# Performance work log

Measured on AMD Instinct MI355X. Metric: run time of the kernel, lower is better.

The kernel has to match this reference:

```python
import jax, jax.numpy as jnp
import numpy as np

N_NODES = 50000
N_EDGES = 1600000
IN_FEAT = 128
OUT_FEAT = 32
N_HEADS = 4
NEG_SLOPE = 0.2


def setup_inputs() -> dict:
    key = jax.random.key(0)
    ks = jax.random.split(key, 7)
    h = jax.random.normal(ks[0], (N_NODES, IN_FEAT), dtype=jnp.float32)
    W = jax.random.normal(ks[1], (IN_FEAT, N_HEADS * OUT_FEAT), dtype=jnp.float32) * 0.05
    attn_l = jax.random.normal(ks[2], (N_HEADS, OUT_FEAT), dtype=jnp.float32) * 0.1
    attn_r = jax.random.normal(ks[3], (N_HEADS, OUT_FEAT), dtype=jnp.float32) * 0.1
    bias = jax.random.normal(ks[4], (N_HEADS * OUT_FEAT,), dtype=jnp.float32) * 0.01
    src = jax.random.randint(ks[5], (N_EDGES,), 0, N_NODES, dtype=jnp.int32)
    dst = jax.random.randint(ks[6], (N_EDGES,), 0, N_NODES, dtype=jnp.int32)
    return {"h": h, "W": W, "attn_l": attn_l, "attn_r": attn_r, "bias": bias, "src": src, "dst": dst}


def reference(h, W, attn_l, attn_r, bias, src, dst):
    N = h.shape[0]
    H, F = attn_l.shape
    # linear projection, [N, H, F]
    feat = (h @ W).reshape(N, H, F)
    # per-node attention halves
    el = jnp.einsum('nhf,hf->nh', feat, attn_l)  # [N, H]
    er = jnp.einsum('nhf,hf->nh', feat, attn_r)  # [N, H]
    # edge scores: e_ij = leaky_relu(el[src] + er[dst])
    e = jax.nn.leaky_relu(el[src] + er[dst], negative_slope=NEG_SLOPE)  # [E, H]
    # edge softmax over incoming edges of each dst node (numerically stable)
    m = jax.ops.segment_max(e, dst, num_segments=N)  # [N, H]
    m = jnp.where(jnp.isfinite(m), m, jnp.zeros_like(m))  # zero-in-degree guard
    ex = jnp.exp(e - m[dst])  # [E, H]
    denom = jax.ops.segment_sum(ex, dst, num_segments=N)  # [N, H]
    alpha = ex / jnp.maximum(denom[dst], 1e-9)  # [E, H]
    # weighted scatter-sum aggregation
    msg = feat[src] * alpha[:, :, None]  # [E, H, F]
    rst = jax.ops.segment_sum(msg, dst, num_segments=N)  # [N, H, F]
    rst = rst + bias.reshape(1, H, F)
    rst = jax.nn.relu(rst)
    # wrapper: norm=None, dropout=0.0 (eval), mean over heads
    return jnp.mean(rst, axis=1)  # [N, F]
```

## Files before the change

kernel.cpp:

```cpp
#include <hip/hip_runtime.h>
#include <hip/hip_bf16.h>
#include <hip/hip_fp16.h>
#include <math.h>


#define NEG_SLOPE 0.2f
#define HEADS 4
#define FEAT_OUT 32
#define FEAT_ALL 128
#define IN_FEAT 128
#define CAP 96
#define KP 136
#define NB_SC 2048

typedef _Float16 half8 __attribute__((ext_vector_type(8)));
typedef float float4v __attribute__((ext_vector_type(4)));
typedef unsigned int uint4v __attribute__((ext_vector_type(4)));

__device__ __forceinline__ float leaky(float v) {
    return v > 0.f ? v : NEG_SLOPE * v;
}

__global__ __launch_bounds__(256) void k1_fused(
    const int* __restrict__ src, const int* __restrict__ dst, int E,
    int* __restrict__ cnt, unsigned short* __restrict__ slots,
    const float* __restrict__ h, const float* __restrict__ W,
    const float* __restrict__ attn_l, const float* __restrict__ attn_r,
    unsigned char* __restrict__ feat8, float2* __restrict__ elsc,
    float* __restrict__ er, int N, int nG) {
    __shared__ _Float16 sf[64 * KP];
    const int t = threadIdx.x;

    if ((int)blockIdx.x >= nG) {
        const int b = blockIdx.x - nG;
        const int p = b & 7;
        const int g = b >> 3;
        const int NPER = (N + 7) >> 3;
        const int lo = p * NPER;
        const int hi = (lo + NPER < N) ? lo + NPER : N;
        const int tpp = (NB_SC >> 3) * 256;
        const int E4 = E & ~3;
        for (int e0 = (g * 256 + t) * 4; e0 < E4; e0 += tpp * 4) {
            uint4v d4 = *(const uint4v*)(dst + e0);
            bool need = false;
#pragma unroll
            for (int j = 0; j < 4; j++)
                need |= ((int)d4[j] >= lo && (int)d4[j] < hi);
            if (!need) continue;
            uint4v s4 = *(const uint4v*)(src + e0);
#pragma unroll
            for (int j = 0; j < 4; j++) {
                int d = (int)d4[j];
                if (d >= lo && d < hi) {
                    int pos = atomicAdd(&cnt[d], 1);
                    if (pos < CAP) slots[(size_t)d * CAP + pos] = (unsigned short)s4[j];
                }
            }
        }
        if (g == 0 && t < E - E4) {
            int e = E4 + t;
            int d = dst[e];
            if (d >= lo && d < hi) {
                int pos = atomicAdd(&cnt[d], 1);
                if (pos < CAP) slots[(size_t)d * CAP + pos] = (unsigned short)src[e];
            }
        }
        return;
    }

    const int n0 = blockIdx.x * 64;
    const int wv_ = t >> 6;
    const int lane = t & 63;
    const int m16 = lane & 15;
    const int quad = lane >> 4;
    const int rowA = wv_ * 16 + m16;
    int nA = n0 + rowA; if (nA > N - 1) nA = N - 1;
    const float* hp = h + (size_t)nA * IN_FEAT + quad * 8;

    float4v acc[8];
#pragma unroll
    for (int i = 0; i < 8; i++) acc[i] = (float4v){0.f, 0.f, 0.f, 0.f};

#pragma unroll
    for (int k0 = 0; k0 < 128; k0 += 32) {
        float4 a0 = *(const float4*)(hp + k0);
        float4 a1 = *(const float4*)(hp + k0 + 4);
        half8 a;
        a[0] = (_Float16)a0.x; a[1] = (_Float16)a0.y;
        a[2] = (_Float16)a0.z; a[3] = (_Float16)a0.w;
        a[4] = (_Float16)a1.x; a[5] = (_Float16)a1.y;
        a[6] = (_Float16)a1.z; a[7] = (_Float16)a1.w;
        const float* wp = W + (size_t)(k0 + quad * 8) * FEAT_ALL + m16;
#pragma unroll
        for (int tN = 0; tN < 8; tN++) {
            const float* wpt = wp + tN * 16;
            half8 b;
            b[0] = (_Float16)wpt[0];
            b[1] = (_Float16)wpt[FEAT_ALL];
            b[2] = (_Float16)wpt[2 * FEAT_ALL];
            b[3] = (_Float16)wpt[3 * FEAT_ALL];
            b[4] = (_Float16)wpt[4 * FEAT_ALL];
            b[5] = (_Float16)wpt[5 * FEAT_ALL];
            b[6] = (_Float16)wpt[6 * FEAT_ALL];
            b[7] = (_Float16)wpt[7 * FEAT_ALL];
            acc[tN] = __builtin_amdgcn_mfma_f32_16x16x32_f16(a, b, acc[tN], 0, 0, 0);
        }
    }

#pragma unroll
    for (int tN = 0; tN < 8; tN++)
#pragma unroll
        for (int r = 0; r < 4; r++) {
            int row = wv_ * 16 + quad * 4 + r;
            sf[row * KP + tN * 16 + m16] = (_Float16)acc[tN][r];
        }
    __syncthreads();

    {
        int r = t >> 2, hh = t & 3;
        int n = n0 + r;
        if (n < N) {
            const _Float16* sp_ = &sf[r * KP + hh * FEAT_OUT];
            float sl = 0.f, sr = 0.f, mx = 0.f;
#pragma unroll
            for (int f = 0; f < FEAT_OUT; f++) {
                float v = (float)sp_[f];
                sl += v * attn_l[hh * FEAT_OUT + f];
                sr += v * attn_r[hh * FEAT_OUT + f];
                mx = fmaxf(mx, fabsf(v));
            }
            er[n * HEADS + hh] = sr;
            elsc[n * HEADS + hh] = make_float2(sl, mx * (1.f / 127.f));
            const float inv = mx > 0.f ? 127.f / mx : 0.f;
            unsigned int w[8];
#pragma unroll
            for (int k2 = 0; k2 < 8; k2++) {
                unsigned int wv = 0;
#pragma unroll
                for (int j = 0; j < 4; j++) {
                    float v = (float)sp_[k2 * 4 + j];
                    int q = __float2int_rn(v * inv);
                    wv |= ((unsigned int)(q & 0xff)) << (8 * j);
                }
                w[k2] = wv;
            }
            uint4* dp = (uint4*)(feat8 + (size_t)n * FEAT_ALL + hh * 32);
            dp[0] = make_uint4(w[0], w[1], w[2], w[3]);
            dp[1] = make_uint4(w[4], w[5], w[6], w[7]);
        }
    }
}

__global__ __launch_bounds__(256) void k5_node(
    const int* __restrict__ cnt, const unsigned short* __restrict__ slots,
    const float2* __restrict__ elsc, const float* __restrict__ er,
    const unsigned char* __restrict__ feat8, const float* __restrict__ bias,
    float* __restrict__ out, int N) {
    const int lane = threadIdx.x & 63;
    const int p = blockIdx.x & 7;
    const int g = blockIdx.x >> 3;
    const int NPER = (N + 7) >> 3;
    const int hi = ((p + 1) * NPER < N) ? (p + 1) * NPER : N;
    const int n = p * NPER + g * 4 + (threadIdx.x >> 6);
    if (n >= hi) return;
    int deg = cnt[n];
    if (deg > CAP) deg = CAP;

    const int sub4 = lane >> 4;
    const int q4 = lane & 15;
    const int hh = q4 >> 2;
    const float ernh = er[n * HEADS + hh];

    float acc[8];
#pragma unroll
    for (int j = 0; j < 8; j++) acc[j] = 0.f;
    float den = 0.f;

    const unsigned short* sp = slots + (size_t)n * CAP;
#pragma unroll 4
    for (int i = sub4; i < deg; i += 4) {
        int s = (int)sp[i];
        float2 es = elsc[s * HEADS + hh];
        float ex = __expf(leaky(es.x + ernh));
        uint2 u = *(const uint2*)(feat8 + (size_t)s * FEAT_ALL + q4 * 8);
        float exs = ex * es.y;
        den += ex;
        union { uint2 v; signed char b[8]; } cv;
        cv.v = u;
        acc[0] += exs * (float)cv.b[0];
        acc[1] += exs * (float)cv.b[1];
        acc[2] += exs * (float)cv.b[2];
        acc[3] += exs * (float)cv.b[3];
        acc[4] += exs * (float)cv.b[4];
        acc[5] += exs * (float)cv.b[5];
        acc[6] += exs * (float)cv.b[6];
        acc[7] += exs * (float)cv.b[7];
    }

#pragma unroll
    for (int j = 0; j < 8; j++) {
        acc[j] += __shfl_xor(acc[j], 16);
        acc[j] += __shfl_xor(acc[j], 32);
    }
    den += __shfl_xor(den, 16);
    den += __shfl_xor(den, 32);
    const float idh = 1.f / fmaxf(den, 1e-9f);

    const float4 b0 = ((const float4*)bias)[q4 * 2];
    const float4 b1 = ((const float4*)bias)[q4 * 2 + 1];
    float v[8];
    v[0] = fmaxf(acc[0] * idh + b0.x, 0.f); v[1] = fmaxf(acc[1] * idh + b0.y, 0.f);
    v[2] = fmaxf(acc[2] * idh + b0.z, 0.f); v[3] = fmaxf(acc[3] * idh + b0.w, 0.f);
    v[4] = fmaxf(acc[4] * idh + b1.x, 0.f); v[5] = fmaxf(acc[5] * idh + b1.y, 0.f);
    v[6] = fmaxf(acc[6] * idh + b1.z, 0.f); v[7] = fmaxf(acc[7] * idh + b1.w, 0.f);
#pragma unroll
    for (int j = 0; j < 8; j++) {
        v[j] += __shfl_xor(v[j], 4);
        v[j] += __shfl_xor(v[j], 8);
    }
    if (lane < 4) {
        float4 o0 = make_float4(v[0] * 0.25f, v[1] * 0.25f, v[2] * 0.25f, v[3] * 0.25f);
        float4 o1 = make_float4(v[4] * 0.25f, v[5] * 0.25f, v[6] * 0.25f, v[7] * 0.25f);
        float* op = out + (size_t)n * FEAT_OUT + lane * 8;
        ((float4*)op)[0] = o0;
        ((float4*)op)[1] = o1;
    }
}

extern "C" void kernel_launch(void* const* d_in, const int* in_sizes, int n_in,
                              void* d_out, int out_size, void* d_ws, size_t ws_size,
                              hipStream_t stream) {
    const float* h      = (const float*)d_in[0];
    const float* W      = (const float*)d_in[1];
    const float* attn_l = (const float*)d_in[2];
    const float* attn_r = (const float*)d_in[3];
    const float* bias   = (const float*)d_in[4];
    const int*   src    = (const int*)d_in[5];
    const int*   dst    = (const int*)d_in[6];
    float* out = (float*)d_out;

    const int N = in_sizes[0] / IN_FEAT;
    const int E = in_sizes[5];

    unsigned char* feat8 = (unsigned char*)d_ws;
    float2* elsc = (float2*)(feat8 + (size_t)N * FEAT_ALL);
    float* er  = (float*)(elsc + (size_t)N * HEADS);
    int* cnt   = (int*)(er + (size_t)N * HEADS);
    unsigned short* slots = (unsigned short*)(cnt + N);

    hipMemsetAsync(cnt, 0, (size_t)N * sizeof(int), stream);

    const int nG = (N + 63) / 64;
    k1_fused<<<nG + NB_SC, 256, 0, stream>>>(src, dst, E, cnt, slots,
                                             h, W, attn_l, attn_r,
                                             feat8, elsc, er, N, nG);

    const int NPER = (N + 7) >> 3;
    const int nb5 = 8 * ((NPER + 3) / 4);
    k5_node<<<nb5, 256, 0, stream>>>(cnt, slots, elsc, er, feat8, bias, out, N);
}
```

Before: 217.8 us.

## Replace per-node atomic slot scatter with two-pass radix bucket sort into CSR

The edge grouping by destination previously used global atomics on per-node counters into fixed-capacity slot arrays. It now packs (src,dst) into one word, builds per-block bucket histograms in shared memory, scans them, places edges into buckets of 128 nodes, and then sorts each bucket locally into a compact CSR. This aims to remove contended global atomics and the padded CAP-sized slot array, but it adds four extra kernel launches and several passes over the edge list. Degree is capped at 255 in the packed row pointer, and the ds-packed layout assumes node ids fit in 16 bits.

```diff
diff --git a/kernel.cpp b/kernel.cpp
--- a/kernel.cpp
+++ b/kernel.cpp
@@ -9,9 +9,9 @@
 #define FEAT_OUT 32
 #define FEAT_ALL 128
 #define IN_FEAT 128
-#define CAP 96
 #define KP 136
-#define NB_SC 2048
+#define NBLK1 512
+#define NBKT_MAX 512
 
 typedef _Float16 half8 __attribute__((ext_vector_type(8)));
 typedef float float4v __attribute__((ext_vector_type(4)));
@@ -23,7 +23,8 @@
 
 __global__ __launch_bounds__(256) void k1_fused(
     const int* __restrict__ src, const int* __restrict__ dst, int E,
-    int* __restrict__ cnt, unsigned short* __restrict__ slots,
+    int che, int nbkt,
+    unsigned int* __restrict__ ds, int* __restrict__ hist,
     const float* __restrict__ h, const float* __restrict__ W,
     const float* __restrict__ attn_l, const float* __restrict__ attn_r,
     unsigned char* __restrict__ feat8, float2* __restrict__ elsc,
@@ -32,39 +33,32 @@
     const int t = threadIdx.x;
 
     if ((int)blockIdx.x >= nG) {
-        const int b = blockIdx.x - nG;
-        const int p = b & 7;
-        const int g = b >> 3;
-        const int NPER = (N + 7) >> 3;
-        const int lo = p * NPER;
-        const int hi = (lo + NPER < N) ? lo + NPER : N;
-        const int tpp = (NB_SC >> 3) * 256;
-        const int E4 = E & ~3;
-        for (int e0 = (g * 256 + t) * 4; e0 < E4; e0 += tpp * 4) {
-            uint4v d4 = *(const uint4v*)(dst + e0);
-            bool need = false;
-#pragma unroll
-            for (int j = 0; j < 4; j++)
-                need |= ((int)d4[j] >= lo && (int)d4[j] < hi);
-            if (!need) continue;
-            uint4v s4 = *(const uint4v*)(src + e0);
-#pragma unroll
-            for (int j = 0; j < 4; j++) {
-                int d = (int)d4[j];
-                if (d >= lo && d < hi) {
-                    int pos = atomicAdd(&cnt[d], 1);
-                    if (pos < CAP) slots[(size_t)d * CAP + pos] = (unsigned short)s4[j];
+        const int blk = blockIdx.x - nG;
+        int* hb = (int*)sf;
+        for (int i = t; i < nbkt; i += 256) hb[i] = 0;
+        __syncthreads();
+        const int e_lo = blk * che;
+        int e_hi = e_lo + che; if (e_hi > E) e_hi = E;
+        for (int e0 = e_lo + t * 4; e0 < e_hi; e0 += 1024) {
+            if (e0 + 3 < e_hi) {
+                uint4v s4 = *(const uint4v*)(src + e0);
+                uint4v d4 = *(const uint4v*)(dst + e0);
+                uint4v r;
+#pragma unroll
+                for (int j = 0; j < 4; j++) r[j] = (s4[j] << 16) | d4[j];
+                *(uint4v*)(ds + e0) = r;
+#pragma unroll
+                for (int j = 0; j < 4; j++) atomicAdd(&hb[d4[j] >> 7], 1);
+            } else {
+                for (int e = e0; e < e_hi; ++e) {
+                    unsigned s = (unsigned)src[e], d = (unsigned)dst[e];
+                    ds[e] = (s << 16) | d;
+                    atomicAdd(&hb[d >> 7], 1);
                 }
             }
         }
-        if (g == 0 && t < E - E4) {
-            int e = E4 + t;
-            int d = dst[e];
-            if (d >= lo && d < hi) {
-                int pos = atomicAdd(&cnt[d], 1);
-                if (pos < CAP) slots[(size_t)d * CAP + pos] = (unsigned short)src[e];
-            }
-        }
+        __syncthreads();
+        for (int i = t; i < nbkt; i += 256) hist[i * NBLK1 + blk] = hb[i];
         return;
     }
 
@@ -151,8 +145,128 @@
     }
 }
 
+__global__ __launch_bounds__(256) void s1_scan(
+    const int* __restrict__ hist, int* __restrict__ base1,
+    int* __restrict__ tot, int nbkt) {
+    __shared__ int sm[256];
+    const int b = blockIdx.x;
+    const int t = threadIdx.x;
+    const int v0 = hist[b * NBLK1 + 2 * t];
+    const int v1 = hist[b * NBLK1 + 2 * t + 1];
+    const int s = v0 + v1;
+    sm[t] = s; __syncthreads();
+    for (int off = 1; off < 256; off <<= 1) {
+        int x = (t >= off) ? sm[t - off] : 0;
+        __syncthreads();
+        sm[t] += x;
+        __syncthreads();
+    }
+    const int excl = sm[t] - s;
+    base1[(2 * t) * nbkt + b] = excl;
+    base1[(2 * t + 1) * nbkt + b] = excl + v0;
+    if (t == 255) tot[b] = sm[255];
+}
+
+__global__ __launch_bounds__(256) void s2_scan(
+    const int* __restrict__ tot, int* __restrict__ bb, int nbkt) {
+    __shared__ int sm[256];
+    const int t = threadIdx.x;
+    const int v0 = (2 * t < nbkt) ? tot[2 * t] : 0;
+    const int v1 = (2 * t + 1 < nbkt) ? tot[2 * t + 1] : 0;
+    const int s = v0 + v1;
+    sm[t] = s; __syncthreads();
+    for (int off = 1; off < 256; off <<= 1) {
+        int x = (t >= off) ? sm[t - off] : 0;
+        __syncthreads();
+        sm[t] += x;
+        __syncthreads();
+    }
+    const int excl = sm[t] - s;
+    if (2 * t <= nbkt) bb[2 * t] = excl;
+    if (2 * t + 1 <= nbkt) bb[2 * t + 1] = excl + v0;
+}
+
+__global__ __launch_bounds__(256) void p2_place(
+    const unsigned int* __restrict__ ds, const int* __restrict__ base1,
+    const int* __restrict__ bb, unsigned int* __restrict__ srt,
+    int E, int che, int nbkt) {
+    __shared__ int cur[NBKT_MAX];
+    const int t = threadIdx.x;
+    const int blk = blockIdx.x;
+    for (int i = t; i < nbkt; i += 256)
+        cur[i] = bb[i] + base1[blk * nbkt + i];
+    __syncthreads();
+    const int e_lo = blk * che;
+    int e_hi = e_lo + che; if (e_hi > E) e_hi = E;
+    for (int e0 = e_lo + t * 4; e0 < e_hi; e0 += 1024) {
+        if (e0 + 3 < e_hi) {
+            uint4v q = *(const uint4v*)(ds + e0);
+#pragma unroll
+            for (int j = 0; j < 4; j++) {
+                int b = (int)(q[j] & 0xffffu) >> 7;
+                int idx = atomicAdd(&cur[b], 1);
+                srt[idx] = q[j];
+            }
+        } else {
+            for (int e = e0; e < e_hi; ++e) {
+                unsigned q = ds[e];
+                int b = (int)(q & 0xffffu) >> 7;
+                int idx = atomicAdd(&cur[b], 1);
+                srt[idx] = q;
+            }
+        }
+    }
+}
+
+__global__ __launch_bounds__(256) void p3_bucket(
+    const unsigned int* __restrict__ srt, const int* __restrict__ bb,
+    unsigned short* __restrict__ slots16, unsigned int* __restrict__ rpd,
+    int N) {
+    __shared__ int h2[128];
+    __shared__ int nbuf[128];
+    const int b = blockIdx.x;
+    const int t = threadIdx.x;
+    const int s0 = bb[b];
+    const int M = bb[b + 1] - s0;
+    const int lo = b << 7;
+    if (t < 128) h2[t] = 0;
+    __syncthreads();
+    for (int i = t; i < M; i += 256) {
+        unsigned q = srt[s0 + i];
+        atomicAdd(&h2[(int)(q & 0xffffu) - lo], 1);
+    }
+    __syncthreads();
+    int hv = 0;
+    if (t < 128) hv = h2[t];
+    for (int off = 1; off < 128; off <<= 1) {
+        int x = 0;
+        if (t < 128 && t >= off) x = h2[t - off];
+        __syncthreads();
+        if (t < 128) h2[t] += x;
+        __syncthreads();
+    }
+    if (t < 128) {
+        const int excl = h2[t] - hv;
+        nbuf[t] = excl;
+        const int n = lo + t;
+        if (n < N) {
+            int dg = hv > 255 ? 255 : hv;
+            rpd[n] = ((unsigned)(s0 + excl) << 8) | (unsigned)dg;
+        }
+    }
+    __syncthreads();
+    if (t < 128) h2[t] = nbuf[t];
+    __syncthreads();
+    for (int i = t; i < M; i += 256) {
+        unsigned q = srt[s0 + i];
+        int n7 = (int)(q & 0xffffu) - lo;
+        int r = atomicAdd(&h2[n7], 1);
+        slots16[s0 + r] = (unsigned short)(q >> 16);
+    }
+}
+
 __global__ __launch_bounds__(256) void k5_node(
-    const int* __restrict__ cnt, const unsigned short* __restrict__ slots,
+    const unsigned int* __restrict__ rpd, const unsigned short* __restrict__ slots16,
     const float2* __restrict__ elsc, const float* __restrict__ er,
     const unsigned char* __restrict__ feat8, const float* __restrict__ bias,
     float* __restrict__ out, int N) {
@@ -163,8 +277,9 @@
     const int hi = ((p + 1) * NPER < N) ? (p + 1) * NPER : N;
     const int n = p * NPER + g * 4 + (threadIdx.x >> 6);
     if (n >= hi) return;
-    int deg = cnt[n];
-    if (deg > CAP) deg = CAP;
+    const unsigned rd = rpd[n];
+    const int deg = (int)(rd & 0xffu);
+    const unsigned short* sp = slots16 + (rd >> 8);
 
     const int sub4 = lane >> 4;
     const int q4 = lane & 15;
@@ -176,7 +291,6 @@
     for (int j = 0; j < 8; j++) acc[j] = 0.f;
     float den = 0.f;
 
-    const unsigned short* sp = slots + (size_t)n * CAP;
 #pragma unroll 4
     for (int i = sub4; i < deg; i += 4) {
         int s = (int)sp[i];
@@ -241,21 +355,33 @@
 
     const int N = in_sizes[0] / IN_FEAT;
     const int E = in_sizes[5];
-
-    unsigned char* feat8 = (unsigned char*)d_ws;
-    float2* elsc = (float2*)(feat8 + (size_t)N * FEAT_ALL);
-    float* er  = (float*)(elsc + (size_t)N * HEADS);
-    int* cnt   = (int*)(er + (size_t)N * HEADS);
-    unsigned short* slots = (unsigned short*)(cnt + N);
-
-    hipMemsetAsync(cnt, 0, (size_t)N * sizeof(int), stream);
+    const int nbkt = (N + 127) >> 7;
+    const int che = (((E + NBLK1 - 1) / NBLK1) + 3) & ~3;
+
+    char* w = (char*)d_ws;
+    auto alloc = [&](size_t bytes) { char* r = w; w += (bytes + 255) & ~(size_t)255; return r; };
+    unsigned char* feat8   = (unsigned char*)alloc((size_t)N * FEAT_ALL);
+    float2*        elsc    = (float2*)alloc((size_t)N * HEADS * sizeof(float2));
+    float*         er      = (float*)alloc((size_t)N * HEADS * sizeof(float));
+    unsigned int*  rpd     = (unsigned int*)alloc((size_t)N * 4);
+    unsigned int*  ds      = (unsigned int*)alloc((size_t)E * 4);
+    unsigned int*  srt     = (unsigned int*)alloc((size_t)E * 4);
+    unsigned short* slots16 = (unsigned short*)alloc((size_t)E * 2);
+    int*           hist    = (int*)alloc((size_t)NBLK1 * nbkt * 4);
+    int*           base1   = (int*)alloc((size_t)NBLK1 * nbkt * 4);
+    int*           tot     = (int*)alloc((size_t)nbkt * 4);
+    int*           bb      = (int*)alloc((size_t)(nbkt + 1) * 4);
 
     const int nG = (N + 63) / 64;
-    k1_fused<<<nG + NB_SC, 256, 0, stream>>>(src, dst, E, cnt, slots,
+    k1_fused<<<nG + NBLK1, 256, 0, stream>>>(src, dst, E, che, nbkt, ds, hist,
                                              h, W, attn_l, attn_r,
                                              feat8, elsc, er, N, nG);
+    s1_scan<<<nbkt, 256, 0, stream>>>(hist, base1, tot, nbkt);
+    s2_scan<<<1, 256, 0, stream>>>(tot, bb, nbkt);
+    p2_place<<<NBLK1, 256, 0, stream>>>(ds, base1, bb, srt, E, che, nbkt);
+    p3_bucket<<<nbkt, 256, 0, stream>>>(srt, bb, slots16, rpd, N);
 
     const int NPER = (N + 7) >> 3;
     const int nb5 = 8 * ((NPER + 3) / 4);
-    k5_node<<<nb5, 256, 0, stream>>>(cnt, slots, elsc, er, feat8, bias, out, N);
-}
+    k5_node<<<nb5, 256, 0, stream>>>(rpd, slots16, elsc, er, feat8, bias, out, N);
+}
```

After: 183.1 us. -16.0%, faster.
